# Performance work log

Measured on AMD Instinct MI355X. Metric: run time of the kernel, lower is better.

Reference implementation:

```python
import jax, jax.numpy as jnp
from jax import lax
import numpy as np

B, COND_C = 16, 256
IN_C, OUT_C, K = 64, 64, 3
H = W = 128
N_PARAM = K * K * IN_C * OUT_C + OUT_C  # 36928


def setup_inputs() -> dict:
    key = jax.random.key(0)
    k1, k2, k3, k4 = jax.random.split(key, 4)
    x = jax.random.normal(k1, (B, IN_C, H, W), dtype=jnp.float32)
    conditioning = jax.random.normal(k2, (B, COND_C), dtype=jnp.float32)
    # nn.Linear(cond_c, n_param): weight [n_param, cond_c], bias [n_param]
    W_cond = jax.random.normal(k3, (N_PARAM, COND_C), dtype=jnp.float32) * 0.02
    b_cond = jax.random.normal(k4, (N_PARAM,), dtype=jnp.float32) * 0.02
    return {"x": x, "conditioning": conditioning, "W_cond": W_cond, "b_cond": b_cond}


def reference(x, conditioning, W_cond, b_cond):
    # Hypernetwork: Linear + tanh*5 (ConditionerActivation)
    w_b = jnp.tanh(conditioning @ W_cond.T + b_cond) * 5.0  # [B, N_PARAM]
    bias = w_b[:, -OUT_C:]                                   # [B, out_c]
    w = w_b[:, :-OUT_C].reshape(B, OUT_C, IN_C, K, K)        # per-sample OIHW

    def conv_one(xi, wi, bi):
        # xi: [in_c, H, W], wi: [out_c, in_c, K, K], bi: [out_c]
        y = lax.conv_general_dilated(
            xi[None], wi,
            window_strides=(1, 1),
            padding=[(1, 1), (1, 1)],
            dimension_numbers=("NCHW", "OIHW", "NCHW"),
        )[0]
        return y + bi[:, None, None]

    return jax.vmap(conv_one)(x, w, bias)  # [B, out_c, H, W]
```

## Files before the change

### kernel.cpp

```cpp
#include <hip/hip_runtime.h>
#include <math.h>
#include <stdint.h>

#define B_    16
#define CONDC 256
#define ICn   64
#define OCn   64
#define Hn    128
#define Wn    128
#define NW    36864
#define NPARAM 36928

typedef _Float16 half8 __attribute__((ext_vector_type(8)));
typedef _Float16 half4 __attribute__((ext_vector_type(4)));
typedef float f32x4 __attribute__((ext_vector_type(4)));
typedef float f32x16 __attribute__((ext_vector_type(16)));

__device__ inline unsigned pk2(float a, float b) {
    union { _Float16 h[2]; unsigned u; } q;
    q.h[0] = (_Float16)a; q.h[1] = (_Float16)b;
    return q.u;
}

__global__ void transpose_k(const float* __restrict__ x, _Float16* __restrict__ xt) {
    __shared__ unsigned ls[4160];
    const int tid = threadIdx.x;
    const int bx  = blockIdx.x;

    if (bx < 2048) {
        const int b = bx >> 7, y = bx & 127;
        const float* xrow = x + (size_t)b * 1048576 + (size_t)y * 128;

        float4 va[4], vb[4];
        #pragma unroll
        for (int t = 0; t < 4; ++t) {
            int u = t * 256 + tid;
            int icp = u >> 5, xg = u & 31;
            const float* r0 = xrow + (size_t)(2 * icp) * 16384;
            va[t] = *((const float4*)r0 + xg);
            vb[t] = *((const float4*)(r0 + 16384) + xg);
        }
        __builtin_amdgcn_sched_barrier(0);

        #pragma unroll
        for (int t = 0; t < 4; ++t) {
            int u = t * 256 + tid;
            int icp = u >> 5, xg = u & 31;
            unsigned* dst = ls + icp * 130 + 4 * xg;
            *(uint2*)(dst)     = make_uint2(pk2(va[t].x, vb[t].x), pk2(va[t].y, vb[t].y));
            *(uint2*)(dst + 2) = make_uint2(pk2(va[t].z, vb[t].z), pk2(va[t].w, vb[t].w));
        }
        __syncthreads();

        _Float16* rowhalf = xt + (size_t)(b * 130 + y + 1) * 8320;
        #pragma unroll
        for (int t = 0; t < 5; ++t) {
            int u = t * 256 + tid;
            if (u < 1040) {
                int xp = u >> 3, g = u & 7;
                uint4 val = make_uint4(0u, 0u, 0u, 0u);
                if (xp > 0 && xp < 129) {
                    int xx = xp - 1;
                    val.x = ls[(4 * g + 0) * 130 + xx];
                    val.y = ls[(4 * g + 1) * 130 + xx];
                    val.z = ls[(4 * g + 2) * 130 + xx];
                    val.w = ls[(4 * g + 3) * 130 + xx];
                }
                *(uint4*)(rowhalf + (size_t)u * 8) = val;
            }
        }
    } else {
        const int q = bx - 2048;
        const int b = q >> 1, yp = (q & 1) ? 129 : 0;
        _Float16* rowhalf = xt + (size_t)(b * 130 + yp) * 8320;
        uint4 z = make_uint4(0u, 0u, 0u, 0u);
        for (int u = tid; u < 1040; u += 256)
            *(uint4*)(rowhalf + (size_t)u * 8) = z;
    }
}

__global__ __launch_bounds__(256, 4) void gemm_k(const float* __restrict__ cond,
                                                 const float* __restrict__ Wc,
                                                 const float* __restrict__ bc,
                                                 _Float16* __restrict__ wt,
                                                 float* __restrict__ bias) {
    __shared__ _Float16 wl[64 * 280];
    const int tid = threadIdx.x;
    const int pbase = blockIdx.x * 64;

    float4 v[16];
    #pragma unroll
    for (int t = 0; t < 16; ++t) {
        int u = t * 256 + tid;
        int pl = u >> 6, kg = u & 63;
        v[t] = *((const float4*)(Wc + (size_t)(pbase + pl) * 256) + kg);
    }
    __builtin_amdgcn_sched_barrier(0);

    #pragma unroll
    for (int t = 0; t < 16; ++t) {
        int u = t * 256 + tid;
        int pl = u >> 6, kg = u & 63;
        half4 h = { (_Float16)v[t].x, (_Float16)v[t].y, (_Float16)v[t].z, (_Float16)v[t].w };
        *(half4*)(wl + pl * 280 + kg * 4) = h;
    }
    __syncthreads();

    const int w = tid >> 6, l = tid & 63, n = l & 15, r4 = l >> 4;
    const _Float16* arow = wl + (w * 16 + n) * 280 + r4 * 8;
    const float*    crow = cond + n * 256 + r4 * 8;
    f32x4 acc = (f32x4){0.f, 0.f, 0.f, 0.f};
    #pragma unroll
    for (int kk = 0; kk < 8; ++kk) {
        half8 av = *(const half8*)(arow + kk * 32);
        float4 u0 = *(const float4*)(crow + kk * 32);
        float4 u1 = *(const float4*)(crow + kk * 32 + 4);
        half8 bv;
        bv[0] = (_Float16)u0.x; bv[1] = (_Float16)u0.y; bv[2] = (_Float16)u0.z; bv[3] = (_Float16)u0.w;
        bv[4] = (_Float16)u1.x; bv[5] = (_Float16)u1.y; bv[6] = (_Float16)u1.z; bv[7] = (_Float16)u1.w;
        acc = __builtin_amdgcn_mfma_f32_16x16x32_f16(av, bv, acc, 0, 0, 0);
    }
    #pragma unroll
    for (int j = 0; j < 4; ++j) {
        int p = pbase + w * 16 + r4 * 4 + j;
        float vv = tanhf(acc[j] + bc[p]) * 5.0f;
        if (p < NW) {
            int oc = p / 576, rem = p - oc * 576;
            int ic = rem / 9,  t  = rem - ic * 9;
            int icq = ic >> 4, icl = ic & 15;
            wt[((((size_t)n * 4 + icq) * 9 + t) * 64 + oc) * 16 + icl] = (_Float16)vv;
        } else {
            bias[n * 64 + (p - NW)] = vv;
        }
    }
}

__global__ __launch_bounds__(256, 3) void conv_v5(const _Float16* __restrict__ xt,
                                                  const _Float16* __restrict__ wt,
                                                  const float* __restrict__ bias,
                                                  float* __restrict__ out) {
    __shared__ _Float16 xs[3 * 6144];
    const int tid = threadIdx.x;
    const int l   = tid & 63;
    const int w   = tid >> 6;
    const int px  = l & 31;
    const int jj  = l >> 5;
    const int ot  = w & 1;
    const int rg  = w >> 1;

    const int sw = (blockIdx.x & 7) * 128 + (blockIdx.x >> 3);
    const int Xt = sw & 3, Yt = (sw >> 2) & 15, b = sw >> 6;
    const int X0  = Xt * 32;
    const int Y0g = Yt * 8;

    const _Float16* xbase = xt + ((size_t)(b * 130 + Y0g) * 130 + X0) * 64;
    const _Float16* wbat  = wt + (size_t)b * 36864 + (size_t)(ot * 32 + px) * 16 + jj * 8;

    int offkw[3];
    #pragma unroll
    for (int kw = 0; kw < 3; ++kw) {
        int c = (px + kw) * 2 + jj;
        offkw[kw] = (c ^ ((c >> 3) & 7)) * 16;
    }
    const int Lb = rg * 4;

    #define STAGEQ(ICQ, BUF) do {                                                       \
        _Pragma("unroll")                                                               \
        for (int it = 0; it < 3; ++it) {                                                \
            int d   = it * 256 + tid;                                                   \
            int row = (int)((unsigned)d / 72u);                                         \
            int c   = d - row * 72;                                                     \
            int cs  = c ^ ((c >> 3) & 7);                                               \
            const _Float16* src = xbase + (size_t)row * 8320 + (cs >> 1) * 64           \
                                + (ICQ) * 16 + (cs & 1) * 8;                            \
            __builtin_amdgcn_global_load_lds(                                           \
                (const __attribute__((address_space(1))) void*)src,                     \
                (__attribute__((address_space(3))) void*)((__attribute__((address_space(3))) char*)xs + (BUF) * 12288 + (it * 256 + (tid & ~63)) * 16), \
                16, 0, 0);                                                              \
        } } while (0)

    #define LOADA(AIDX, ICQ) do {                                                       \
        _Pragma("unroll")                                                               \
        for (int t = 0; t < 9; ++t)                                                     \
            A[AIDX][t] = *(const half8*)(wbat + (size_t)((ICQ) * 9 + t) * 1024);        \
        } while (0)

    #define COMPUTE(AIDX, BUF) do {                                                     \
        const char* bufb = (const char*)xs + (BUF) * 12288;                             \
        _Pragma("unroll")                                                               \
        for (int kw = 0; kw < 3; ++kw) {                                                \
            half8 Bf[6];                                                                \
            _Pragma("unroll")                                                           \
            for (int iy = 0; iy < 6; ++iy)                                              \
                Bf[iy] = *(const half8*)(bufb + (Lb + iy) * 1152 + offkw[kw]);          \
            _Pragma("unroll")                                                           \
            for (int iy = 0; iy < 6; ++iy) {                                            \
                _Pragma("unroll")                                                       \
                for (int kh = 0; kh < 3; ++kh) {                                        \
                    const int r = iy - kh;                                              \
                    if (r >= 0 && r < 4)                                                \
                        acc[r] = __builtin_amdgcn_mfma_f32_32x32x16_f16(A[AIDX][kh * 3 + kw], Bf[iy], acc[r], 0, 0, 0); \
                } } } } while (0)

    half8 A[2][9];
    f32x16 acc[4];
    #pragma unroll
    for (int r = 0; r < 4; ++r) acc[r] = (f32x16){};

    LOADA(0, 0);
    __builtin_amdgcn_sched_barrier(0);
    STAGEQ(0, 0); STAGEQ(1, 1); STAGEQ(2, 2);
    __builtin_amdgcn_sched_barrier(0);

    LOADA(1, 1);
    __builtin_amdgcn_sched_barrier(0);
    asm volatile("s_waitcnt vmcnt(15)" ::: "memory");
    __builtin_amdgcn_sched_barrier(0);
    __builtin_amdgcn_s_barrier();
    __builtin_amdgcn_sched_barrier(0);
    COMPUTE(0, 0);
    asm volatile("s_waitcnt lgkmcnt(0)" ::: "memory");
    __builtin_amdgcn_sched_barrier(0);
    __builtin_amdgcn_s_barrier();
    __builtin_amdgcn_sched_barrier(0);
    STAGEQ(3, 0);
    __builtin_amdgcn_sched_barrier(0);

    LOADA(0, 2);
    __builtin_amdgcn_sched_barrier(0);
    asm volatile("s_waitcnt vmcnt(12)" ::: "memory");
    __builtin_amdgcn_sched_barrier(0);
    __builtin_amdgcn_s_barrier();
    __builtin_amdgcn_sched_barrier(0);
    COMPUTE(1, 1);

    LOADA(1, 3);
    __builtin_amdgcn_sched_barrier(0);
    asm volatile("s_waitcnt vmcnt(9)" ::: "memory");
    __builtin_amdgcn_sched_barrier(0);
    __builtin_amdgcn_s_barrier();
    __builtin_amdgcn_sched_barrier(0);
    COMPUTE(0, 2);

    asm volatile("s_waitcnt vmcnt(0)" ::: "memory");
    __builtin_amdgcn_sched_barrier(0);
    __builtin_amdgcn_s_barrier();
    __builtin_amdgcn_sched_barrier(0);
    COMPUTE(1, 0);

    #undef STAGEQ
    #undef LOADA
    #undef COMPUTE

    const float* bb = bias + b * 64;
    #pragma unroll
    for (int r = 0; r < 4; ++r) {
        const int yo = Y0g + Lb + r;
        float* ob = out + (((size_t)(b * 64 + ot * 32)) * 128 + yo) * 128 + X0 + px;
        #pragma unroll
        for (int reg = 0; reg < 16; ++reg) {
            const int ocl = (reg & 3) + 8 * (reg >> 2) + 4 * jj;
            ob[(size_t)ocl * 16384] = acc[r][reg] + bb[ot * 32 + ocl];
        }
    }
}

__global__ __launch_bounds__(256) void cond_gemm(const float* __restrict__ cond,
                                                 const float* __restrict__ Wc,
                                                 const float* __restrict__ bc,
                                                 float* __restrict__ wb) {
    __shared__ float condl[B_][CONDC + 1];
    __shared__ float Wl[16][CONDC + 1];
    const int tid = threadIdx.x;
    const int p0 = blockIdx.x * 16;
    for (int i = tid; i < B_ * CONDC; i += 256) condl[i >> 8][i & 255] = cond[i];
    for (int i = tid; i < 16 * CONDC; i += 256) {
        int pl = i >> 8, k = i & 255;
        Wl[pl][k] = Wc[(p0 + pl) * CONDC + k];
    }
    __syncthreads();
    const int pl = tid >> 4;
    const int b  = tid & 15;
    float acc = bc[p0 + pl];
    #pragma unroll 8
    for (int k = 0; k < CONDC; ++k) acc += Wl[pl][k] * condl[b][k];
    wb[b * NPARAM + p0 + pl] = tanhf(acc) * 5.0f;
}

#define TS  32
#define OG  8
#define ICC 8
__global__ __launch_bounds__(256) void conv_kernel(const float* __restrict__ x,
                                                   const float* __restrict__ wb,
                                                   float* __restrict__ out) {
    __shared__ float fxs[ICC][TS + 2][TS + 2];
    __shared__ float ws[OG][ICC][9];
    const int tid = threadIdx.x;
    const int b   = blockIdx.z;
    const int ocg = blockIdx.y * OG;
    const int tx0 = (blockIdx.x & 3) * TS;
    const int ty0 = (blockIdx.x >> 2) * TS;
    const int px  = (tid & 15) * 2;
    const int py  = (tid >> 4) * 2;
    float acc[OG][4];
    #pragma unroll
    for (int o = 0; o < OG; ++o)
        #pragma unroll
        for (int q = 0; q < 4; ++q) acc[o][q] = 0.0f;
    const float* wbase = wb + b * NPARAM;
    for (int ic0 = 0; ic0 < ICn; ic0 += ICC) {
        for (int i = tid; i < ICC * (TS + 2) * (TS + 2); i += 256) {
            int icl = i / ((TS + 2) * (TS + 2));
            int rem = i % ((TS + 2) * (TS + 2));
            int yy = rem / (TS + 2), xx = rem % (TS + 2);
            int gy = ty0 - 1 + yy, gx = tx0 - 1 + xx;
            float v = 0.0f;
            if (gy >= 0 && gy < Hn && gx >= 0 && gx < Wn)
                v = x[((b * ICn + ic0 + icl) * Hn + gy) * Wn + gx];
            fxs[icl][yy][xx] = v;
        }
        for (int i = tid; i < OG * ICC * 9; i += 256) {
            int o = i / (ICC * 9), rem = i % (ICC * 9);
            int icl = rem / 9, k = rem % 9;
            ws[o][icl][k] = wbase[((ocg + o) * ICn + ic0 + icl) * 9 + k];
        }
        __syncthreads();
        #pragma unroll
        for (int icl = 0; icl < ICC; ++icl) {
            float xv[4][4];
            #pragma unroll
            for (int dy = 0; dy < 4; ++dy)
                #pragma unroll
                for (int dx = 0; dx < 4; ++dx) xv[dy][dx] = fxs[icl][py + dy][px + dx];
            #pragma unroll
            for (int o = 0; o < OG; ++o)
                #pragma unroll
                for (int kh = 0; kh < 3; ++kh)
                    #pragma unroll
                    for (int kw = 0; kw < 3; ++kw) {
                        float wv = ws[o][icl][kh * 3 + kw];
                        acc[o][0] += xv[kh][kw] * wv;
                        acc[o][1] += xv[kh][kw + 1] * wv;
                        acc[o][2] += xv[kh + 1][kw] * wv;
                        acc[o][3] += xv[kh + 1][kw + 1] * wv;
                    }
        }
        __syncthreads();
    }
    #pragma unroll
    for (int o = 0; o < OG; ++o) {
        float bias = wbase[NW + ocg + o];
        int oc = ocg + o;
        float* obase = out + ((size_t)(b * OCn + oc) * Hn + (ty0 + py)) * Wn + tx0 + px;
        obase[0] = acc[o][0] + bias;
        obase[1] = acc[o][1] + bias;
        obase[Wn] = acc[o][2] + bias;
        obase[Wn + 1] = acc[o][3] + bias;
    }
}

extern "C" void kernel_launch(void* const* d_in, const int* in_sizes, int n_in,
                              void* d_out, int out_size, void* d_ws, size_t ws_size,
                              hipStream_t stream) {
    const float* x    = (const float*)d_in[0];
    const float* cond = (const float*)d_in[1];
    const float* Wc   = (const float*)d_in[2];
    const float* bc   = (const float*)d_in[3];
    float* out = (float*)d_out;

    const size_t WT_BYTES = (size_t)B_ * 9 * 64 * 64 * 2;
    const size_t BIAS_OFF = WT_BYTES;
    const size_t XT_OFF   = 1183744;
    const size_t XT_BYTES = (size_t)B_ * 130 * 130 * 64 * 2 + 32768;
    const size_t NEED     = XT_OFF + XT_BYTES;

    if (ws_size >= NEED) {
        _Float16* wt   = (_Float16*)d_ws;
        float*    bias = (float*)((char*)d_ws + BIAS_OFF);
        _Float16* xt   = (_Float16*)((char*)d_ws + XT_OFF);
        transpose_k<<<dim3(2048 + 32), 256, 0, stream>>>(x, xt);
        gemm_k<<<dim3(577), 256, 0, stream>>>(cond, Wc, bc, wt, bias);
        conv_v5<<<dim3(1024), 256, 0, stream>>>(xt, wt, bias, out);
    } else {
        float* wbuf = (float*)d_ws;
        cond_gemm<<<dim3(NPARAM / 16), 256, 0, stream>>>(cond, Wc, bc, wbuf);
        conv_kernel<<<dim3(16, OCn / OG, B_), 256, 0, stream>>>(x, wbuf, out);
    }
}
```

Measured before the change: 62.77 us.

## Merge transpose and hypernet GEMM kernels; load conv weights inline at higher occupancy

The input transpose/pad kernel and the hypernetwork GEMM now run as one launch, with blocks picking their role by block index. This removes a kernel launch and lets the two independent prep jobs overlap. The conv kernel no longer preloads the 18 weight fragments per stage into registers. It reads each fragment from global memory right at the MFMA instead, which lowers register pressure so launch bounds can go from 3 to 4 waves. The trade-off is that weight loads now sit on the MFMA critical path without being hidden, and the vmcnt waits were recounted to match.

```diff
diff --git a/kernel.cpp b/kernel.cpp
--- a/kernel.cpp
+++ b/kernel.cpp
@@ -22,14 +22,21 @@
     return q.u;
 }
 
-__global__ void transpose_k(const float* __restrict__ x, _Float16* __restrict__ xt) {
-    __shared__ unsigned ls[4160];
+__global__ void prep2(const float* __restrict__ x,
+                      const float* __restrict__ cond,
+                      const float* __restrict__ Wc,
+                      const float* __restrict__ bc,
+                      _Float16* __restrict__ xt,
+                      _Float16* __restrict__ wt,
+                      float* __restrict__ bias) {
+    __shared__ unsigned smem[8960];
     const int tid = threadIdx.x;
     const int bx  = blockIdx.x;
 
     if (bx < 2048) {
         const int b = bx >> 7, y = bx & 127;
         const float* xrow = x + (size_t)b * 1048576 + (size_t)y * 128;
+        unsigned* ls = smem;
 
         float4 va[4], vb[4];
         #pragma unroll
@@ -69,73 +76,66 @@
                 *(uint4*)(rowhalf + (size_t)u * 8) = val;
             }
         }
-    } else {
+    } else if (bx < 2080) {
         const int q = bx - 2048;
         const int b = q >> 1, yp = (q & 1) ? 129 : 0;
         _Float16* rowhalf = xt + (size_t)(b * 130 + yp) * 8320;
         uint4 z = make_uint4(0u, 0u, 0u, 0u);
         for (int u = tid; u < 1040; u += 256)
             *(uint4*)(rowhalf + (size_t)u * 8) = z;
-    }
-}
-
-__global__ __launch_bounds__(256, 4) void gemm_k(const float* __restrict__ cond,
-                                                 const float* __restrict__ Wc,
-                                                 const float* __restrict__ bc,
-                                                 _Float16* __restrict__ wt,
-                                                 float* __restrict__ bias) {
-    __shared__ _Float16 wl[64 * 280];
-    const int tid = threadIdx.x;
-    const int pbase = blockIdx.x * 64;
-
-    float4 v[16];
-    #pragma unroll
-    for (int t = 0; t < 16; ++t) {
-        int u = t * 256 + tid;
-        int pl = u >> 6, kg = u & 63;
-        v[t] = *((const float4*)(Wc + (size_t)(pbase + pl) * 256) + kg);
-    }
-    __builtin_amdgcn_sched_barrier(0);
-
-    #pragma unroll
-    for (int t = 0; t < 16; ++t) {
-        int u = t * 256 + tid;
-        int pl = u >> 6, kg = u & 63;
-        half4 h = { (_Float16)v[t].x, (_Float16)v[t].y, (_Float16)v[t].z, (_Float16)v[t].w };
-        *(half4*)(wl + pl * 280 + kg * 4) = h;
-    }
-    __syncthreads();
-
-    const int w = tid >> 6, l = tid & 63, n = l & 15, r4 = l >> 4;
-    const _Float16* arow = wl + (w * 16 + n) * 280 + r4 * 8;
-    const float*    crow = cond + n * 256 + r4 * 8;
-    f32x4 acc = (f32x4){0.f, 0.f, 0.f, 0.f};
-    #pragma unroll
-    for (int kk = 0; kk < 8; ++kk) {
-        half8 av = *(const half8*)(arow + kk * 32);
-        float4 u0 = *(const float4*)(crow + kk * 32);
-        float4 u1 = *(const float4*)(crow + kk * 32 + 4);
-        half8 bv;
-        bv[0] = (_Float16)u0.x; bv[1] = (_Float16)u0.y; bv[2] = (_Float16)u0.z; bv[3] = (_Float16)u0.w;
-        bv[4] = (_Float16)u1.x; bv[5] = (_Float16)u1.y; bv[6] = (_Float16)u1.z; bv[7] = (_Float16)u1.w;
-        acc = __builtin_amdgcn_mfma_f32_16x16x32_f16(av, bv, acc, 0, 0, 0);
-    }
-    #pragma unroll
-    for (int j = 0; j < 4; ++j) {
-        int p = pbase + w * 16 + r4 * 4 + j;
-        float vv = tanhf(acc[j] + bc[p]) * 5.0f;
-        if (p < NW) {
-            int oc = p / 576, rem = p - oc * 576;
-            int ic = rem / 9,  t  = rem - ic * 9;
-            int icq = ic >> 4, icl = ic & 15;
-            wt[((((size_t)n * 4 + icq) * 9 + t) * 64 + oc) * 16 + icl] = (_Float16)vv;
-        } else {
-            bias[n * 64 + (p - NW)] = vv;
-        }
-    }
-}
-
-__global__ __launch_bounds__(256, 3) void conv_v5(const _Float16* __restrict__ xt,
+    } else {
+        const int pbase = (bx - 2080) * 64;
+        _Float16* wl = (_Float16*)smem;
+
+        float4 v[16];
+        #pragma unroll
+        for (int t = 0; t < 16; ++t) {
+            int u = t * 256 + tid;
+            int pl = u >> 6, kg = u & 63;
+            v[t] = *((const float4*)(Wc + (size_t)(pbase + pl) * 256) + kg);
+        }
+        __builtin_amdgcn_sched_barrier(0);
+
+        #pragma unroll
+        for (int t = 0; t < 16; ++t) {
+            int u = t * 256 + tid;
+            int pl = u >> 6, kg = u & 63;
+            half4 h = { (_Float16)v[t].x, (_Float16)v[t].y, (_Float16)v[t].z, (_Float16)v[t].w };
+            *(half4*)(wl + pl * 280 + kg * 4) = h;
+        }
+        __syncthreads();
+
+        const int w = tid >> 6, l = tid & 63, n = l & 15, r4 = l >> 4;
+        const _Float16* arow = wl + (w * 16 + n) * 280 + r4 * 8;
+        const float*    crow = cond + n * 256 + r4 * 8;
+        f32x4 acc = (f32x4){0.f, 0.f, 0.f, 0.f};
+        #pragma unroll
+        for (int kk = 0; kk < 8; ++kk) {
+            half8 av = *(const half8*)(arow + kk * 32);
+            float4 u0 = *(const float4*)(crow + kk * 32);
+            float4 u1 = *(const float4*)(crow + kk * 32 + 4);
+            half8 bv;
+            bv[0] = (_Float16)u0.x; bv[1] = (_Float16)u0.y; bv[2] = (_Float16)u0.z; bv[3] = (_Float16)u0.w;
+            bv[4] = (_Float16)u1.x; bv[5] = (_Float16)u1.y; bv[6] = (_Float16)u1.z; bv[7] = (_Float16)u1.w;
+            acc = __builtin_amdgcn_mfma_f32_16x16x32_f16(av, bv, acc, 0, 0, 0);
+        }
+        #pragma unroll
+        for (int j = 0; j < 4; ++j) {
+            int p = pbase + w * 16 + r4 * 4 + j;
+            float vv = tanhf(acc[j] + bc[p]) * 5.0f;
+            if (p < NW) {
+                int oc = p / 576, rem = p - oc * 576;
+                int ic = rem / 9,  t  = rem - ic * 9;
+                int icq = ic >> 4, icl = ic & 15;
+                wt[((((size_t)n * 4 + icq) * 9 + t) * 64 + oc) * 16 + icl] = (_Float16)vv;
+            } else {
+                bias[n * 64 + (p - NW)] = vv;
+            }
+        }
+    }
+}
+
+__global__ __launch_bounds__(256, 4) void conv_v7(const _Float16* __restrict__ xt,
                                                   const _Float16* __restrict__ wt,
                                                   const float* __restrict__ bias,
                                                   float* __restrict__ out) {
@@ -179,14 +179,9 @@
                 16, 0, 0);                                                              \
         } } while (0)
 
-    #define LOADA(AIDX, ICQ) do {                                                       \
-        _Pragma("unroll")                                                               \
-        for (int t = 0; t < 9; ++t)                                                     \
-            A[AIDX][t] = *(const half8*)(wbat + (size_t)((ICQ) * 9 + t) * 1024);        \
-        } while (0)
-
-    #define COMPUTE(AIDX, BUF) do {                                                     \
+    #define COMPUTE(ICQ, BUF) do {                                                      \
         const char* bufb = (const char*)xs + (BUF) * 12288;                             \
+        const _Float16* wq = wbat + (size_t)(ICQ) * 9216;                               \
         _Pragma("unroll")                                                               \
         for (int kw = 0; kw < 3; ++kw) {                                                \
             half8 Bf[6];                                                                \
@@ -199,22 +194,18 @@
                 for (int kh = 0; kh < 3; ++kh) {                                        \
                     const int r = iy - kh;                                              \
                     if (r >= 0 && r < 4)                                                \
-                        acc[r] = __builtin_amdgcn_mfma_f32_32x32x16_f16(A[AIDX][kh * 3 + kw], Bf[iy], acc[r], 0, 0, 0); \
+                        acc[r] = __builtin_amdgcn_mfma_f32_32x32x16_f16(                \
+                            *(const half8*)(wq + (kh * 3 + kw) * 1024), Bf[iy], acc[r], 0, 0, 0); \
                 } } } } while (0)
 
-    half8 A[2][9];
     f32x16 acc[4];
     #pragma unroll
     for (int r = 0; r < 4; ++r) acc[r] = (f32x16){};
 
-    LOADA(0, 0);
-    __builtin_amdgcn_sched_barrier(0);
     STAGEQ(0, 0); STAGEQ(1, 1); STAGEQ(2, 2);
     __builtin_amdgcn_sched_barrier(0);
 
-    LOADA(1, 1);
-    __builtin_amdgcn_sched_barrier(0);
-    asm volatile("s_waitcnt vmcnt(15)" ::: "memory");
+    asm volatile("s_waitcnt vmcnt(6)" ::: "memory");
     __builtin_amdgcn_sched_barrier(0);
     __builtin_amdgcn_s_barrier();
     __builtin_amdgcn_sched_barrier(0);
@@ -226,30 +217,25 @@
     STAGEQ(3, 0);
     __builtin_amdgcn_sched_barrier(0);
 
-    LOADA(0, 2);
-    __builtin_amdgcn_sched_barrier(0);
-    asm volatile("s_waitcnt vmcnt(12)" ::: "memory");
+    asm volatile("s_waitcnt vmcnt(6)" ::: "memory");
     __builtin_amdgcn_sched_barrier(0);
     __builtin_amdgcn_s_barrier();
     __builtin_amdgcn_sched_barrier(0);
     COMPUTE(1, 1);
 
-    LOADA(1, 3);
-    __builtin_amdgcn_sched_barrier(0);
-    asm volatile("s_waitcnt vmcnt(9)" ::: "memory");
-    __builtin_amdgcn_sched_barrier(0);
-    __builtin_amdgcn_s_barrier();
-    __builtin_amdgcn_sched_barrier(0);
-    COMPUTE(0, 2);
+    asm volatile("s_waitcnt vmcnt(3)" ::: "memory");
+    __builtin_amdgcn_sched_barrier(0);
+    __builtin_amdgcn_s_barrier();
+    __builtin_amdgcn_sched_barrier(0);
+    COMPUTE(2, 2);
 
     asm volatile("s_waitcnt vmcnt(0)" ::: "memory");
     __builtin_amdgcn_sched_barrier(0);
     __builtin_amdgcn_s_barrier();
     __builtin_amdgcn_sched_barrier(0);
-    COMPUTE(1, 0);
+    COMPUTE(3, 0);
 
     #undef STAGEQ
-    #undef LOADA
     #undef COMPUTE
 
     const float* bb = bias + b * 64;
@@ -378,9 +364,8 @@
         _Float16* wt   = (_Float16*)d_ws;
         float*    bias = (float*)((char*)d_ws + BIAS_OFF);
         _Float16* xt   = (_Float16*)((char*)d_ws + XT_OFF);
-        transpose_k<<<dim3(2048 + 32), 256, 0, stream>>>(x, xt);
-        gemm_k<<<dim3(577), 256, 0, stream>>>(cond, Wc, bc, wt, bias);
-        conv_v5<<<dim3(1024), 256, 0, stream>>>(xt, wt, bias, out);
+        prep2<<<dim3(2048 + 32 + 577), 256, 0, stream>>>(x, cond, Wc, bc, xt, wt, bias);
+        conv_v7<<<dim3(1024), 256, 0, stream>>>(xt, wt, bias, out);
     } else {
         float* wbuf = (float*)d_ws;
         cond_gemm<<<dim3(NPARAM / 16), 256, 0, stream>>>(cond, Wc, bc, wbuf);
```

Result: slower. 64.95 us (+3.5%).
